# Kernel tuning notes

Hardware: AMD Instinct MI355X
Metric: run time of the kernel (lower is better)

Reference implementation:

```python
import jax, jax.numpy as jnp
import numpy as np

B, N, D, H = 8, 1024, 768, 4
ALPHA = 0.2      # LeakyReLU negative slope in GraphAttentionLayer
NEG = -9e15      # mask fill value for non-edges (pyGAT convention)


def setup_inputs() -> dict:
    key = jax.random.key(0)
    ks = jax.random.split(key, 8)
    input_emb = jax.random.normal(ks[0], (B, N, D), jnp.float32)
    adj = jax.random.randint(ks[1], (B, N, N), 0, 2, dtype=jnp.int32)
    mask_node = jnp.ones((B, N), jnp.float32)
    s = 1.0 / np.sqrt(D).astype(np.float32)
    W_heads = jax.random.normal(ks[2], (H, D, D), jnp.float32) * s          # per-head W: nfeat->nhid
    a_heads = jax.random.normal(ks[3], (H, 2 * D, 1), jnp.float32) * s      # per-head attention vector a
    W_out = jax.random.normal(ks[4], (H * D, D), jnp.float32) * (1.0 / np.sqrt(H * D).astype(np.float32))
    a_out = jax.random.normal(ks[5], (2 * D, 1), jnp.float32) * s
    w_cls = jax.random.normal(ks[6], (D, 1), jnp.float32) * s               # Classifier.linear1 weight
    b_cls = jnp.zeros((1,), jnp.float32)
    return dict(input_emb=input_emb, adj=adj, mask_node=mask_node,
                W_heads=W_heads, a_heads=a_heads, W_out=W_out, a_out=a_out,
                w_cls=w_cls, b_cls=b_cls)


def _gat_layer(x, adj_mask, W, a, concat):
    # x: [B,N,Fin], W: [Fin,Fout], a: [2*Fout,1], adj_mask: [B,N,N] bool
    Wh = jnp.einsum('bnd,df->bnf', x, W)            # [B,N,Fout]
    Fo = W.shape[1]
    f1 = Wh @ a[:Fo]                                 # [B,N,1] source term
    f2 = Wh @ a[Fo:]                                 # [B,N,1] target term
    e = jax.nn.leaky_relu(f1 + jnp.swapaxes(f2, 1, 2), ALPHA)  # [B,N,N]
    e = jnp.where(adj_mask, e, NEG)
    att = jax.nn.softmax(e, axis=-1)                 # dropout=0 -> no attention dropout
    h = jnp.einsum('bij,bjf->bif', att, Wh)          # [B,N,Fout]
    return jax.nn.elu(h) if concat else h


def reference(input_emb, adj, mask_node, W_heads, a_heads, W_out, a_out, w_cls, b_cls):
    adj_mask = adj > 0
    # multi-head GAT (concat=True heads), vectorized over heads and batch
    heads = jax.vmap(lambda Wi, ai: _gat_layer(input_emb, adj_mask, Wi, ai, True))(W_heads, a_heads)  # [H,B,N,D]
    xx = jnp.moveaxis(heads, 0, 2).reshape(B, N, H * D)  # torch.cat over heads, dim=1 per node
    out = jax.nn.elu(_gat_layer(xx, adj_mask, W_out, a_out, False))
    # dropout_layer(p=0.5) assumed eval mode (identity); residual add
    yy = out + input_emb                               # [B,N,D]
    h = (yy @ w_cls + b_cls)[..., 0]                   # Classifier linear -> [B,N]
    node_scores = jax.nn.sigmoid(h) * mask_node
    return yy, node_scores
```

## Files before the change

kernel.cpp:

```cpp
#include <hip/hip_runtime.h>


typedef unsigned short ushortT;
typedef _Float16 f16;
typedef __attribute__((ext_vector_type(8))) _Float16 f16x8;
typedef __attribute__((ext_vector_type(4))) _Float16 f16x4;
typedef __attribute__((ext_vector_type(4))) float f32x4;
typedef __attribute__((ext_vector_type(2))) float f32x2;
typedef __attribute__((ext_vector_type(8))) unsigned short u16x8;
typedef __attribute__((ext_vector_type(2))) unsigned short u16x2;
typedef __attribute__((ext_vector_type(4))) int i32x4;

#define ALPHA 0.2f

__device__ __forceinline__ float b2f(ushortT u) {
  union { unsigned int i; float f; } c; c.i = ((unsigned int)u) << 16; return c.f;
}
__device__ __forceinline__ ushortT f2b(float f) {
  union { float f; unsigned int u; } c; c.f = f;
  unsigned int u = c.u;
  u += 0x7FFFu + ((u >> 16) & 1u);
  return (ushortT)(u >> 16);
}

__global__ void detect_dtype(const ushortT* __restrict__ X, int* __restrict__ flag,
                             float* __restrict__ fvec) {
  __shared__ int s[256];
  int t = threadIdx.x, c = 0;
  for (int i = t; i < 2048; i += 256) fvec[i] = 0.f;
  for (int i = t; i < 16384; i += 256) {
    int e = (X[2 * i] >> 7) & 0xFF;
    if (e > 140 || e < 100) c++;
  }
  s[t] = c; __syncthreads();
  for (int o = 128; o > 0; o >>= 1) { if (t < o) s[t] += s[t + o]; __syncthreads(); }
  if (t == 0) *flag = (s[0] > 1000) ? 1 : 0;
}

template <int MODE, int BSRC>
__global__ __launch_bounds__(256) void mgemm(
    const void* __restrict__ Ab, const void* __restrict__ Bb,
    void* __restrict__ Cb, const void* __restrict__ Rb,
    int K, int lda, int ldb, int aRaw,
    long aOff, long bOff, long cOff, long rOff, int accum,
    const void* __restrict__ avec, long avOff, int fd, float* __restrict__ fvec,
    int zf, const int* __restrict__ rflag) {
  __shared__ __align__(16) f16 As[2][64 * 64];
  __shared__ __align__(16) f16 Bs[2][64 * 64];
  int t = threadIdx.x;
  int n0 = blockIdx.x * 64, m0 = blockIdx.y * 64;
  int flg = *rflag;
  int aTy = aRaw ? (flg ? 2 : 1) : 0;

  if (zf && blockIdx.x == 0 && blockIdx.y == 0) {
#pragma unroll
    for (int i = 0; i < 8; i++) fvec[t + i * 256] = 0.f;
  }

  int tq = t >> 2, cq = t & 3;
  long aBase = aOff + (long)(m0 + tq) * lda + cq * 16;
  int stA0 = tq * 64 + (((2 * cq)     ^ (tq & 7)) * 8);
  int stA1 = tq * 64 + (((2 * cq + 1) ^ (tq & 7)) * 8);

  const f16*     Ah = (const f16*)Ab;
  const ushortT* Au = (const ushortT*)Ab;
  const float*   Af = (const float*)Ab;
  const f16*     Bh = (const f16*)Bb;
  const ushortT* Bu = (const ushortT*)Bb;
  const float*   Bf = (const float*)Bb;

  long bBase = 0;
  int stB0, stB1;
  int q2 = 0, cB = 0;
  if (BSRC == 0) {
    bBase = bOff + (long)(n0 + tq) * (long)K + cq * 16;
    stB0 = stA0; stB1 = stA1;
  } else {
    q2 = t & 31; cB = t >> 5;
    int nb0 = 2 * q2, nb1 = nb0 + 1;
    stB0 = nb0 * 64 + ((cB ^ (nb0 & 7)) * 8);
    stB1 = nb1 * 64 + ((cB ^ (nb1 & 7)) * 8);
  }

  f16x8 ra0, ra1, rb0, rb1;

  auto loadA = [&](int kt) {
    long g = aBase + (long)kt * 64;
    if (aTy == 0) {
      ra0 = *(const f16x8*)(Ah + g);
      ra1 = *(const f16x8*)(Ah + g + 8);
    } else if (aTy == 1) {
      u16x8 v0 = *(const u16x8*)(Au + g);
      u16x8 v1 = *(const u16x8*)(Au + g + 8);
#pragma unroll
      for (int j = 0; j < 8; j++) { ra0[j] = (f16)b2f(v0[j]); ra1[j] = (f16)b2f(v1[j]); }
    } else {
      f32x4 v0 = *(const f32x4*)(Af + g);
      f32x4 v1 = *(const f32x4*)(Af + g + 4);
      f32x4 v2 = *(const f32x4*)(Af + g + 8);
      f32x4 v3 = *(const f32x4*)(Af + g + 12);
#pragma unroll
      for (int j = 0; j < 4; j++) {
        ra0[j] = (f16)v0[j]; ra0[4 + j] = (f16)v1[j];
        ra1[j] = (f16)v2[j]; ra1[4 + j] = (f16)v3[j];
      }
    }
  };
  auto loadB = [&](int kt) {
    if (BSRC == 0) {
      long g = bBase + (long)kt * 64;
      rb0 = *(const f16x8*)(Bh + g);
      rb1 = *(const f16x8*)(Bh + g + 8);
    } else {
      long rbase = bOff + (long)(kt * 64 + cB * 8) * ldb + n0 + 2 * q2;
      if (flg) {
#pragma unroll
        for (int j = 0; j < 8; j++) {
          f32x2 v = *(const f32x2*)(Bf + rbase + (long)j * ldb);
          rb0[j] = (f16)v[0]; rb1[j] = (f16)v[1];
        }
      } else {
#pragma unroll
        for (int j = 0; j < 8; j++) {
          u16x2 v = *(const u16x2*)(Bu + rbase + (long)j * ldb);
          rb0[j] = (f16)b2f(v[0]); rb1[j] = (f16)b2f(v[1]);
        }
      }
    }
  };
  auto stage = [&](int buf) {
    *(f16x8*)(&As[buf][0] + stA0) = ra0;  *(f16x8*)(&As[buf][0] + stA1) = ra1;
    *(f16x8*)(&Bs[buf][0] + stB0) = rb0;  *(f16x8*)(&Bs[buf][0] + stB1) = rb1;
  };

  int lane = t & 63, wid = t >> 6;
  int wr = wid >> 1, wc = wid & 1;
  int lr = lane & 15, lg = lane >> 4, l7 = lane & 7;
  int aRow0 = (wr * 32 + lr) * 64, aRow1 = aRow0 + 16 * 64;
  int bRow0 = (wc * 32 + lr) * 64, bRow1 = bRow0 + 16 * 64;
  int ch0 = ((lg) ^ l7) * 8, ch1 = ((4 + lg) ^ l7) * 8;

  f32x4 acc[2][2];
#pragma unroll
  for (int i = 0; i < 2; i++)
#pragma unroll
    for (int j = 0; j < 2; j++) acc[i][j] = (f32x4){0.f, 0.f, 0.f, 0.f};

  int KT = K >> 6;
  loadA(0); loadB(0);
  stage(0);
  loadA(1); loadB(1);
  __syncthreads();

  for (int kt = 0; kt < KT; ++kt) {
    int cur = kt & 1;
    if (kt + 1 < KT) stage(cur ^ 1);
    if (kt + 2 < KT) { loadA(kt + 2); loadB(kt + 2); }
#pragma unroll
    for (int kk = 0; kk < 2; kk++) {
      int ch = kk ? ch1 : ch0;
      f16x8 a0 = *(const f16x8*)(&As[cur][0] + aRow0 + ch);
      f16x8 a1 = *(const f16x8*)(&As[cur][0] + aRow1 + ch);
      f16x8 b0 = *(const f16x8*)(&Bs[cur][0] + bRow0 + ch);
      f16x8 b1 = *(const f16x8*)(&Bs[cur][0] + bRow1 + ch);
      acc[0][0] = __builtin_amdgcn_mfma_f32_16x16x32_f16(a0, b0, acc[0][0], 0, 0, 0);
      acc[0][1] = __builtin_amdgcn_mfma_f32_16x16x32_f16(a0, b1, acc[0][1], 0, 0, 0);
      acc[1][0] = __builtin_amdgcn_mfma_f32_16x16x32_f16(a1, b0, acc[1][0], 0, 0, 0);
      acc[1][1] = __builtin_amdgcn_mfma_f32_16x16x32_f16(a1, b1, acc[1][1], 0, 0, 0);
    }
    __syncthreads();
  }

  int rowb_base = m0 + wr * 32 + 4 * lg;
  int col_base  = n0 + wc * 32 + lr;

  float a1v[2], a2v[2];
  float p1[2][4], p2[2][4];
  if (fd) {
    const float* avf = (const float*)avec; const ushortT* avu = (const ushortT*)avec;
#pragma unroll
    for (int fn = 0; fn < 2; fn++) {
      int c = n0 + wc * 32 + fn * 16 + lr;
      a1v[fn] = flg ? avf[avOff + c]       : b2f(avu[avOff + c]);
      a2v[fn] = flg ? avf[avOff + 768 + c] : b2f(avu[avOff + 768 + c]);
    }
#pragma unroll
    for (int fm = 0; fm < 2; fm++)
#pragma unroll
      for (int r = 0; r < 4; r++) { p1[fm][r] = 0.f; p2[fm][r] = 0.f; }
  }

#pragma unroll
  for (int fm = 0; fm < 2; fm++) {
#pragma unroll
    for (int fn = 0; fn < 2; fn++) {
      int rowb = rowb_base + fm * 16;
      int col  = col_base + fn * 16;
      f32x4 v = acc[fm][fn];
      float fullv[4];
      if (MODE == 4) {
        f16x4 pk;
#pragma unroll
        for (int r = 0; r < 4; r++) { fullv[r] = v[r]; pk[r] = (f16)v[r]; }
        *(f16x4*)((f16*)Cb + (long)col * 1024 + rowb) = pk;
      } else if (MODE == 3) {
        f16* Cc = (f16*)Cb;
        long idx = (long)col * 1024 + rowb;
        f16x4 pk;
        if (accum) {
          f16x4 old = *(const f16x4*)(Cc + idx);
#pragma unroll
          for (int r = 0; r < 4; r++) { fullv[r] = (float)old[r] + v[r]; pk[r] = (f16)fullv[r]; }
        } else {
#pragma unroll
          for (int r = 0; r < 4; r++) { fullv[r] = v[r]; pk[r] = (f16)v[r]; }
        }
        *(f16x4*)(Cc + idx) = pk;
      } else {
#pragma unroll
        for (int r = 0; r < 4; r++) {
          int row = rowb + r;
          float x = v[r];
          x = x > 0.f ? x : __expf(x) - 1.f;
          long ci = cOff + (long)row * 768 + col;
          if (MODE == 2) {
            long ri = rOff + (long)row * 768 + col;
            x += flg ? ((const float*)Rb)[ri] : b2f(((const ushortT*)Rb)[ri]);
            if (flg) ((float*)Cb)[ci] = x;
            else     ((ushortT*)Cb)[ci] = f2b(x);
          } else {
            ((f16*)Cb)[ci] = (f16)x;
          }
        }
      }
      if (fd) {
        float ac1 = a1v[fn], ac2 = a2v[fn];
#pragma unroll
        for (int r = 0; r < 4; r++) {
          p1[fm][r] += fullv[r] * ac1;
          p2[fm][r] += fullv[r] * ac2;
        }
      }
    }
  }

  if (fd) {
#pragma unroll
    for (int fm = 0; fm < 2; fm++)
#pragma unroll
      for (int r = 0; r < 4; r++) {
#pragma unroll
        for (int o = 1; o < 16; o <<= 1) {
          p1[fm][r] += __shfl_xor(p1[fm][r], o);
          p2[fm][r] += __shfl_xor(p2[fm][r], o);
        }
      }
    if (lr == 0) {
#pragma unroll
      for (int fm = 0; fm < 2; fm++)
#pragma unroll
        for (int r = 0; r < 4; r++) {
          int row = rowb_base + fm * 16 + r;
          atomicAdd(fvec + row, p1[fm][r]);
          atomicAdd(fvec + 1024 + row, p2[fm][r]);
        }
    }
  }
}

__global__ __launch_bounds__(256) void attn_kernel(
    const float* __restrict__ f1, const float* __restrict__ f2,
    const int* __restrict__ adj, f16* __restrict__ att) {
  __shared__ float sred[8];
  int i = blockIdx.x;
  const int* arow = adj + (size_t)i * 1024;
  float f1i = f1[i];
  f16* orow = att + (size_t)i * 1024;
  int t = threadIdx.x, lane = t & 63, wid = t >> 6;
  int j0 = t * 4;

  i32x4 av = *(const i32x4*)(arow + j0);
  f32x4 fv = *(const f32x4*)(f2 + j0);

  float e[4];
  int msk[4];
  float mx = -1e38f;
#pragma unroll
  for (int c = 0; c < 4; c++) {
    float ev = f1i + fv[c];
    ev = ev > 0.f ? ev : ALPHA * ev;
    e[c] = ev;
    msk[c] = av[c] > 0;
    if (msk[c]) mx = fmaxf(mx, ev);
  }
#pragma unroll
  for (int o = 32; o > 0; o >>= 1) mx = fmaxf(mx, __shfl_down(mx, o));
  if (lane == 0) sred[wid] = mx;
  __syncthreads();
  float bmx = fmaxf(fmaxf(sred[0], sred[1]), fmaxf(sred[2], sred[3]));
  bool none = bmx < -1e37f;

  float p[4];
  float sum = 0.f;
#pragma unroll
  for (int c = 0; c < 4; c++) {
    p[c] = none ? 1.f : (msk[c] ? __expf(e[c] - bmx) : 0.f);
    sum += p[c];
  }
#pragma unroll
  for (int o = 32; o > 0; o >>= 1) sum += __shfl_down(sum, o);
  if (lane == 0) sred[4 + wid] = sum;
  __syncthreads();
  float inv = 1.f / (sred[4] + sred[5] + sred[6] + sred[7]);
  f16x4 pk;
#pragma unroll
  for (int c = 0; c < 4; c++) pk[c] = (f16)(p[c] * inv);
  *(f16x4*)(orow + j0) = pk;
}

__global__ __launch_bounds__(256) void cls_kernel(
    void* __restrict__ outbase, const void* __restrict__ w,
    const void* __restrict__ bc, const void* __restrict__ mask,
    const int* __restrict__ rflag) {
  int t = threadIdx.x, lane = t & 63, wv = t >> 6;
  long row = (long)blockIdx.x * 4 + wv;
  int f32 = *rflag;
  const float* yf = (const float*)outbase; const ushortT* yu = (const ushortT*)outbase;
  const float* wf = (const float*)w;       const ushortT* wu = (const ushortT*)w;
  float s = 0.f;
  for (int d = lane; d < 768; d += 64) {
    float yv = f32 ? yf[row * 768 + d] : b2f(yu[row * 768 + d]);
    float wvv = f32 ? wf[d] : b2f(wu[d]);
    s += yv * wvv;
  }
#pragma unroll
  for (int o = 32; o > 0; o >>= 1) s += __shfl_down(s, o);
  if (lane == 0) {
    float bb = f32 ? ((const float*)bc)[0] : b2f(((const ushortT*)bc)[0]);
    float mk = f32 ? ((const float*)mask)[row] : b2f(((const ushortT*)mask)[row]);
    float sig = 1.f / (1.f + __expf(-(s + bb)));
    long oi = 6291456L + row;
    if (f32) ((float*)outbase)[oi] = sig * mk;
    else ((ushortT*)outbase)[oi] = f2b(sig * mk);
  }
}

extern "C" void kernel_launch(void* const* d_in, const int* in_sizes, int n_in,
                              void* d_out, int out_size, void* d_ws, size_t ws_size,
                              hipStream_t stream) {
  (void)in_sizes; (void)n_in; (void)out_size; (void)ws_size;

  const void* X    = d_in[0];
  const int*  adj  = (const int*)d_in[1];
  const void* maskN= d_in[2];
  const void* Wh   = d_in[3];
  const void* aH   = d_in[4];
  const void* Wo   = d_in[5];
  const void* aO   = d_in[6];
  const void* wcls = d_in[7];
  const void* bcls = d_in[8];

  char* ws = (char*)d_ws;
  float* f1   = (float*)(ws + 0);
  float* f2   = (float*)(ws + 4096);
  int*   flag = (int*)(ws + 8192);
  f16* Wh1T = (f16*)(ws + 8448);
  f16* Wh2T = (f16*)(ws + 1581312);
  f16* attb = (f16*)(ws + 3154176);
  f16* hout = (f16*)(ws + 5251328);

  detect_dtype<<<1, 256, 0, stream>>>((const ushortT*)X, flag, f1);

  dim3 gg(12, 16);
  for (int b = 0; b < 8; b++) {
    long xOff = (long)b * 786432;
    for (int h = 0; h < 4; h++) {
      mgemm<4, 1><<<gg, 256, 0, stream>>>(
          X, Wh, Wh1T, nullptr, 768, 768, 768, 1,
          xOff, (long)h * 589824, 0L, 0L, 0, aH, (long)h * 1536, 1, f1, 0, flag);
      attn_kernel<<<1024, 256, 0, stream>>>(f1, f2, adj + (size_t)b * 1048576, attb);
      mgemm<1, 0><<<gg, 256, 0, stream>>>(
          attb, Wh1T, hout, nullptr, 1024, 1024, 0, 0,
          0L, 0L, 0L, 0L, 0, nullptr, 0L, 0, f1, 1, flag);
      mgemm<3, 1><<<gg, 256, 0, stream>>>(
          hout, Wo, Wh2T, nullptr, 768, 768, 768, 0,
          0L, (long)h * 589824, 0L, 0L, h > 0 ? 1 : 0, aO, 0L, h == 3 ? 1 : 0, f1, 0, flag);
    }
    attn_kernel<<<1024, 256, 0, stream>>>(f1, f2, adj + (size_t)b * 1048576, attb);
    mgemm<2, 0><<<gg, 256, 0, stream>>>(
        attb, Wh2T, d_out, X, 1024, 1024, 0, 0,
        0L, 0L, xOff, xOff, 0, nullptr, 0L, 0, f1, 1, flag);
  }

  cls_kernel<<<2048, 256, 0, stream>>>(d_out, wcls, bcls, maskN, flag);
}
```

Baseline: 1.779 ms.

## Pair independent GEMMs into single launches and use direct global-to-LDS loads

Independent GEMMs now share one launch through a z grid dimension: each head's Wo projection runs alongside the next head's Wh projection, and each batch's final attention GEMM runs alongside the next batch's first Wh projection. This is meant to fill the GPU better than the small 192-block grids did and to cut launch count. To keep the paired GEMMs from clobbering each other's f1/f2 scores, those vectors are double-buffered, with the second buffer placed in a scratch region past the outputs in d_out. The f16 A/B GEMM path also switches to global_load_lds with a swizzled layout, skipping the register staging. The risks are reliance on spare space in the output buffer and the more complex zeroing and phase logic.

```diff
diff --git a/kernel.cpp b/kernel.cpp
--- a/kernel.cpp
+++ b/kernel.cpp
@@ -22,116 +22,65 @@
   u += 0x7FFFu + ((u >> 16) & 1u);
   return (ushortT)(u >> 16);
 }
+__device__ __forceinline__ float* qbuf(char* dout, int flg) {
+  return (float*)(dout + (flg ? 25165824L : 12582912L));
+}
+__device__ __forceinline__ void gld16(const f16* g, f16* l) {
+  __builtin_amdgcn_global_load_lds(
+      (const __attribute__((address_space(1))) void*)g,
+      (__attribute__((address_space(3))) void*)l, 16, 0, 0);
+}
 
 __global__ void detect_dtype(const ushortT* __restrict__ X, int* __restrict__ flag,
-                             float* __restrict__ fvec) {
+                             float* __restrict__ Pws, char* __restrict__ dout) {
   __shared__ int s[256];
   int t = threadIdx.x, c = 0;
-  for (int i = t; i < 2048; i += 256) fvec[i] = 0.f;
   for (int i = t; i < 16384; i += 256) {
     int e = (X[2 * i] >> 7) & 0xFF;
     if (e > 140 || e < 100) c++;
   }
   s[t] = c; __syncthreads();
   for (int o = 128; o > 0; o >>= 1) { if (t < o) s[t] += s[t + o]; __syncthreads(); }
-  if (t == 0) *flag = (s[0] > 1000) ? 1 : 0;
-}
+  __syncthreads();
+  int fl = (s[0] > 1000) ? 1 : 0;
+  if (t == 0) *flag = fl;
+  float* Qv = qbuf(dout, fl);
+#pragma unroll
+  for (int i = 0; i < 8; i++) { Pws[t + i * 256] = 0.f; Qv[t + i * 256] = 0.f; }
+}
+
+struct GA {
+  const void* A; const void* B; void* C; const void* R; const void* avec;
+  long aOff, bOff, cOff, rOff, avOff;
+  int K, lda, ldb, aRaw, accum, fd, fsel, zmask;
+};
 
 template <int MODE, int BSRC>
-__global__ __launch_bounds__(256) void mgemm(
-    const void* __restrict__ Ab, const void* __restrict__ Bb,
-    void* __restrict__ Cb, const void* __restrict__ Rb,
-    int K, int lda, int ldb, int aRaw,
-    long aOff, long bOff, long cOff, long rOff, int accum,
-    const void* __restrict__ avec, long avOff, int fd, float* __restrict__ fvec,
-    int zf, const int* __restrict__ rflag) {
-  __shared__ __align__(16) f16 As[2][64 * 64];
-  __shared__ __align__(16) f16 Bs[2][64 * 64];
+__device__ void gbody(const GA a, float* Pws, char* dout, int flg,
+                      f16* AS, f16* BS) {
   int t = threadIdx.x;
   int n0 = blockIdx.x * 64, m0 = blockIdx.y * 64;
-  int flg = *rflag;
-  int aTy = aRaw ? (flg ? 2 : 1) : 0;
-
-  if (zf && blockIdx.x == 0 && blockIdx.y == 0) {
-#pragma unroll
-    for (int i = 0; i < 8; i++) fvec[t + i * 256] = 0.f;
-  }
-
-  int tq = t >> 2, cq = t & 3;
-  long aBase = aOff + (long)(m0 + tq) * lda + cq * 16;
-  int stA0 = tq * 64 + (((2 * cq)     ^ (tq & 7)) * 8);
-  int stA1 = tq * 64 + (((2 * cq + 1) ^ (tq & 7)) * 8);
-
-  const f16*     Ah = (const f16*)Ab;
-  const ushortT* Au = (const ushortT*)Ab;
-  const float*   Af = (const float*)Ab;
-  const f16*     Bh = (const f16*)Bb;
-  const ushortT* Bu = (const ushortT*)Bb;
-  const float*   Bf = (const float*)Bb;
-
-  long bBase = 0;
-  int stB0, stB1;
-  int q2 = 0, cB = 0;
-  if (BSRC == 0) {
-    bBase = bOff + (long)(n0 + tq) * (long)K + cq * 16;
-    stB0 = stA0; stB1 = stA1;
-  } else {
-    q2 = t & 31; cB = t >> 5;
-    int nb0 = 2 * q2, nb1 = nb0 + 1;
-    stB0 = nb0 * 64 + ((cB ^ (nb0 & 7)) * 8);
-    stB1 = nb1 * 64 + ((cB ^ (nb1 & 7)) * 8);
-  }
-
-  f16x8 ra0, ra1, rb0, rb1;
-
-  auto loadA = [&](int kt) {
-    long g = aBase + (long)kt * 64;
-    if (aTy == 0) {
-      ra0 = *(const f16x8*)(Ah + g);
-      ra1 = *(const f16x8*)(Ah + g + 8);
-    } else if (aTy == 1) {
-      u16x8 v0 = *(const u16x8*)(Au + g);
-      u16x8 v1 = *(const u16x8*)(Au + g + 8);
-#pragma unroll
-      for (int j = 0; j < 8; j++) { ra0[j] = (f16)b2f(v0[j]); ra1[j] = (f16)b2f(v1[j]); }
-    } else {
-      f32x4 v0 = *(const f32x4*)(Af + g);
-      f32x4 v1 = *(const f32x4*)(Af + g + 4);
-      f32x4 v2 = *(const f32x4*)(Af + g + 8);
-      f32x4 v3 = *(const f32x4*)(Af + g + 12);
-#pragma unroll
-      for (int j = 0; j < 4; j++) {
-        ra0[j] = (f16)v0[j]; ra0[4 + j] = (f16)v1[j];
-        ra1[j] = (f16)v2[j]; ra1[4 + j] = (f16)v3[j];
-      }
-    }
-  };
-  auto loadB = [&](int kt) {
-    if (BSRC == 0) {
-      long g = bBase + (long)kt * 64;
-      rb0 = *(const f16x8*)(Bh + g);
-      rb1 = *(const f16x8*)(Bh + g + 8);
-    } else {
-      long rbase = bOff + (long)(kt * 64 + cB * 8) * ldb + n0 + 2 * q2;
-      if (flg) {
-#pragma unroll
-        for (int j = 0; j < 8; j++) {
-          f32x2 v = *(const f32x2*)(Bf + rbase + (long)j * ldb);
-          rb0[j] = (f16)v[0]; rb1[j] = (f16)v[1];
-        }
-      } else {
-#pragma unroll
-        for (int j = 0; j < 8; j++) {
-          u16x2 v = *(const u16x2*)(Bu + rbase + (long)j * ldb);
-          rb0[j] = (f16)b2f(v[0]); rb1[j] = (f16)b2f(v[1]);
-        }
-      }
-    }
-  };
-  auto stage = [&](int buf) {
-    *(f16x8*)(&As[buf][0] + stA0) = ra0;  *(f16x8*)(&As[buf][0] + stA1) = ra1;
-    *(f16x8*)(&Bs[buf][0] + stB0) = rb0;  *(f16x8*)(&Bs[buf][0] + stB1) = rb1;
-  };
+  int aTy = a.aRaw ? (flg ? 2 : 1) : 0;
+  float* fv = a.fsel ? qbuf(dout, flg) : Pws;
+
+  if (a.zmask && blockIdx.x == 0 && blockIdx.y == 0) {
+    if (a.zmask & 1) {
+#pragma unroll
+      for (int i = 0; i < 8; i++) Pws[t + i * 256] = 0.f;
+    }
+    if (a.zmask & 2) {
+      float* Qv = qbuf(dout, flg);
+#pragma unroll
+      for (int i = 0; i < 8; i++) Qv[t + i * 256] = 0.f;
+    }
+  }
+
+  const f16*     Ah = (const f16*)a.A;
+  const ushortT* Au = (const ushortT*)a.A;
+  const float*   Af = (const float*)a.A;
+  const f16*     Bh = (const f16*)a.B;
+  const ushortT* Bu = (const ushortT*)a.B;
+  const float*   Bf = (const float*)a.B;
 
   int lane = t & 63, wid = t >> 6;
   int wr = wid >> 1, wc = wid & 1;
@@ -146,29 +95,118 @@
 #pragma unroll
     for (int j = 0; j < 2; j++) acc[i][j] = (f32x4){0.f, 0.f, 0.f, 0.f};
 
-  int KT = K >> 6;
-  loadA(0); loadB(0);
-  stage(0);
-  loadA(1); loadB(1);
-  __syncthreads();
-
-  for (int kt = 0; kt < KT; ++kt) {
-    int cur = kt & 1;
-    if (kt + 1 < KT) stage(cur ^ 1);
-    if (kt + 2 < KT) { loadA(kt + 2); loadB(kt + 2); }
+  auto compute = [&](int cur) {
+    f16* Ac = AS + cur * 4096; f16* Bc = BS + cur * 4096;
 #pragma unroll
     for (int kk = 0; kk < 2; kk++) {
       int ch = kk ? ch1 : ch0;
-      f16x8 a0 = *(const f16x8*)(&As[cur][0] + aRow0 + ch);
-      f16x8 a1 = *(const f16x8*)(&As[cur][0] + aRow1 + ch);
-      f16x8 b0 = *(const f16x8*)(&Bs[cur][0] + bRow0 + ch);
-      f16x8 b1 = *(const f16x8*)(&Bs[cur][0] + bRow1 + ch);
+      f16x8 a0 = *(const f16x8*)(Ac + aRow0 + ch);
+      f16x8 a1 = *(const f16x8*)(Ac + aRow1 + ch);
+      f16x8 b0 = *(const f16x8*)(Bc + bRow0 + ch);
+      f16x8 b1 = *(const f16x8*)(Bc + bRow1 + ch);
       acc[0][0] = __builtin_amdgcn_mfma_f32_16x16x32_f16(a0, b0, acc[0][0], 0, 0, 0);
       acc[0][1] = __builtin_amdgcn_mfma_f32_16x16x32_f16(a0, b1, acc[0][1], 0, 0, 0);
       acc[1][0] = __builtin_amdgcn_mfma_f32_16x16x32_f16(a1, b0, acc[1][0], 0, 0, 0);
       acc[1][1] = __builtin_amdgcn_mfma_f32_16x16x32_f16(a1, b1, acc[1][1], 0, 0, 0);
     }
+  };
+
+  int KT = a.K >> 6;
+
+  if (BSRC == 0) {
+    int gr = lane >> 3, gcn = lane & 7, swz = (gcn ^ (gr & 7)) * 8;
+    int isB = wid >> 1, cq4 = (wid & 1) * 4;
+    long gA = a.aOff + (long)(m0 + gr) * a.lda + swz;
+    long gB = a.bOff + (long)(n0 + gr) * (long)a.K + swz;
+    auto stageG = [&](int buf, int kt) {
+      if (!isB) {
+        const f16* g = Ah + gA + (long)kt * 64;
+        f16* dst = AS + buf * 4096;
+#pragma unroll
+        for (int c = 0; c < 4; c++)
+          gld16(g + (long)(cq4 + c) * 8 * a.lda, dst + (cq4 + c) * 512);
+      } else {
+        const f16* g = Bh + gB + (long)kt * 64;
+        f16* dst = BS + buf * 4096;
+#pragma unroll
+        for (int c = 0; c < 4; c++)
+          gld16(g + (long)(cq4 + c) * 8 * a.K, dst + (cq4 + c) * 512);
+      }
+    };
+    stageG(0, 0);
     __syncthreads();
+    for (int kt = 0; kt < KT; ++kt) {
+      int cur = kt & 1;
+      if (kt + 1 < KT) stageG(cur ^ 1, kt + 1);
+      compute(cur);
+      __syncthreads();
+    }
+  } else {
+    int tq = t >> 2, cq = t & 3;
+    long aBase = a.aOff + (long)(m0 + tq) * a.lda + cq * 16;
+    int stA0 = tq * 64 + (((2 * cq)     ^ (tq & 7)) * 8);
+    int stA1 = tq * 64 + (((2 * cq + 1) ^ (tq & 7)) * 8);
+    int q2 = t & 31, cB = t >> 5;
+    int nb0 = 2 * q2, nb1 = nb0 + 1;
+    int stB0 = nb0 * 64 + ((cB ^ (nb0 & 7)) * 8);
+    int stB1 = nb1 * 64 + ((cB ^ (nb1 & 7)) * 8);
+
+    f16x8 ra0, ra1, rb0, rb1;
+    auto loadA = [&](int kt) {
+      long g = aBase + (long)kt * 64;
+      if (aTy == 0) {
+        ra0 = *(const f16x8*)(Ah + g);
+        ra1 = *(const f16x8*)(Ah + g + 8);
+      } else if (aTy == 1) {
+        u16x8 v0 = *(const u16x8*)(Au + g);
+        u16x8 v1 = *(const u16x8*)(Au + g + 8);
+#pragma unroll
+        for (int j = 0; j < 8; j++) { ra0[j] = (f16)b2f(v0[j]); ra1[j] = (f16)b2f(v1[j]); }
+      } else {
+        f32x4 v0 = *(const f32x4*)(Af + g);
+        f32x4 v1 = *(const f32x4*)(Af + g + 4);
+        f32x4 v2 = *(const f32x4*)(Af + g + 8);
+        f32x4 v3 = *(const f32x4*)(Af + g + 12);
+#pragma unroll
+        for (int j = 0; j < 4; j++) {
+          ra0[j] = (f16)v0[j]; ra0[4 + j] = (f16)v1[j];
+          ra1[j] = (f16)v2[j]; ra1[4 + j] = (f16)v3[j];
+        }
+      }
+    };
+    auto loadB = [&](int kt) {
+      long rbase = a.bOff + (long)(kt * 64 + cB * 8) * a.ldb + n0 + 2 * q2;
+      if (flg) {
+#pragma unroll
+        for (int j = 0; j < 8; j++) {
+          f32x2 v = *(const f32x2*)(Bf + rbase + (long)j * a.ldb);
+          rb0[j] = (f16)v[0]; rb1[j] = (f16)v[1];
+        }
+      } else {
+#pragma unroll
+        for (int j = 0; j < 8; j++) {
+          u16x2 v = *(const u16x2*)(Bu + rbase + (long)j * a.ldb);
+          rb0[j] = (f16)b2f(v[0]); rb1[j] = (f16)b2f(v[1]);
+        }
+      }
+    };
+    auto stage = [&](int buf) {
+      *(f16x8*)(AS + buf * 4096 + stA0) = ra0;
+      *(f16x8*)(AS + buf * 4096 + stA1) = ra1;
+      *(f16x8*)(BS + buf * 4096 + stB0) = rb0;
+      *(f16x8*)(BS + buf * 4096 + stB1) = rb1;
+    };
+    loadA(0); loadB(0);
+    stage(0);
+    loadA(1); loadB(1);
+    __syncthreads();
+    for (int kt = 0; kt < KT; ++kt) {
+      int cur = kt & 1;
+      if (kt + 1 < KT) stage(cur ^ 1);
+      if (kt + 2 < KT) { loadA(kt + 2); loadB(kt + 2); }
+      compute(cur);
+      __syncthreads();
+    }
   }
 
   int rowb_base = m0 + wr * 32 + 4 * lg;
@@ -176,13 +214,13 @@
 
   float a1v[2], a2v[2];
   float p1[2][4], p2[2][4];
-  if (fd) {
-    const float* avf = (const float*)avec; const ushortT* avu = (const ushortT*)avec;
+  if (a.fd) {
+    const float* avf = (const float*)a.avec; const ushortT* avu = (const ushortT*)a.avec;
 #pragma unroll
     for (int fn = 0; fn < 2; fn++) {
       int c = n0 + wc * 32 + fn * 16 + lr;
-      a1v[fn] = flg ? avf[avOff + c]       : b2f(avu[avOff + c]);
-      a2v[fn] = flg ? avf[avOff + 768 + c] : b2f(avu[avOff + 768 + c]);
+      a1v[fn] = flg ? avf[a.avOff + c]       : b2f(avu[a.avOff + c]);
+      a2v[fn] = flg ? avf[a.avOff + 768 + c] : b2f(avu[a.avOff + 768 + c]);
     }
 #pragma unroll
     for (int fm = 0; fm < 2; fm++)
@@ -202,12 +240,12 @@
         f16x4 pk;
 #pragma unroll
         for (int r = 0; r < 4; r++) { fullv[r] = v[r]; pk[r] = (f16)v[r]; }
-        *(f16x4*)((f16*)Cb + (long)col * 1024 + rowb) = pk;
+        *(f16x4*)((f16*)a.C + (long)col * 1024 + rowb) = pk;
       } else if (MODE == 3) {
-        f16* Cc = (f16*)Cb;
+        f16* Cc = (f16*)a.C;
         long idx = (long)col * 1024 + rowb;
         f16x4 pk;
-        if (accum) {
+        if (a.accum) {
           f16x4 old = *(const f16x4*)(Cc + idx);
 #pragma unroll
           for (int r = 0; r < 4; r++) { fullv[r] = (float)old[r] + v[r]; pk[r] = (f16)fullv[r]; }
@@ -222,18 +260,18 @@
           int row = rowb + r;
           float x = v[r];
           x = x > 0.f ? x : __expf(x) - 1.f;
-          long ci = cOff + (long)row * 768 + col;
+          long ci = a.cOff + (long)row * 768 + col;
           if (MODE == 2) {
-            long ri = rOff + (long)row * 768 + col;
-            x += flg ? ((const float*)Rb)[ri] : b2f(((const ushortT*)Rb)[ri]);
-            if (flg) ((float*)Cb)[ci] = x;
-            else     ((ushortT*)Cb)[ci] = f2b(x);
+            long ri = a.rOff + (long)row * 768 + col;
+            x += flg ? ((const float*)a.R)[ri] : b2f(((const ushortT*)a.R)[ri]);
+            if (flg) ((float*)a.C)[ci] = x;
+            else     ((ushortT*)a.C)[ci] = f2b(x);
           } else {
-            ((f16*)Cb)[ci] = (f16)x;
+            ((f16*)a.C)[ci] = (f16)x;
           }
         }
       }
-      if (fd) {
+      if (a.fd) {
         float ac1 = a1v[fn], ac2 = a2v[fn];
 #pragma unroll
         for (int r = 0; r < 4; r++) {
@@ -244,7 +282,7 @@
     }
   }
 
-  if (fd) {
+  if (a.fd) {
 #pragma unroll
     for (int fm = 0; fm < 2; fm++)
 #pragma unroll
@@ -261,17 +299,46 @@
 #pragma unroll
         for (int r = 0; r < 4; r++) {
           int row = rowb_base + fm * 16 + r;
-          atomicAdd(fvec + row, p1[fm][r]);
-          atomicAdd(fvec + 1024 + row, p2[fm][r]);
-        }
-    }
-  }
+          atomicAdd(fv + row, p1[fm][r]);
+          atomicAdd(fv + 1024 + row, p2[fm][r]);
+        }
+    }
+  }
+}
+
+template <int MODE, int BSRC>
+__global__ __launch_bounds__(256) void k_solo(GA a, float* Pws, char* dout,
+                                              const int* __restrict__ rflag) {
+  __shared__ __align__(16) f16 As[2][4096];
+  __shared__ __align__(16) f16 Bs[2][4096];
+  gbody<MODE, BSRC>(a, Pws, dout, *rflag, &As[0][0], &Bs[0][0]);
+}
+__global__ __launch_bounds__(256) void k_pair31(GA g3, GA g1, float* Pws, char* dout,
+                                                const int* __restrict__ rflag) {
+  __shared__ __align__(16) f16 As[2][4096];
+  __shared__ __align__(16) f16 Bs[2][4096];
+  int flg = *rflag;
+  if (blockIdx.z == 0) gbody<3, 1>(g3, Pws, dout, flg, &As[0][0], &Bs[0][0]);
+  else                 gbody<4, 1>(g1, Pws, dout, flg, &As[0][0], &Bs[0][0]);
+}
+__global__ __launch_bounds__(256) void k_pair41(GA g4, GA g1, float* Pws, char* dout,
+                                                const int* __restrict__ rflag) {
+  __shared__ __align__(16) f16 As[2][4096];
+  __shared__ __align__(16) f16 Bs[2][4096];
+  int flg = *rflag;
+  if (blockIdx.z == 0) gbody<2, 0>(g4, Pws, dout, flg, &As[0][0], &Bs[0][0]);
+  else                 gbody<4, 1>(g1, Pws, dout, flg, &As[0][0], &Bs[0][0]);
 }
 
 __global__ __launch_bounds__(256) void attn_kernel(
-    const float* __restrict__ f1, const float* __restrict__ f2,
-    const int* __restrict__ adj, f16* __restrict__ att) {
+    const float* __restrict__ Pws, char* __restrict__ dout, int fsel,
+    const int* __restrict__ adj, f16* __restrict__ att,
+    const int* __restrict__ rflag) {
   __shared__ float sred[8];
+  int flg = *rflag;
+  const float* fvb = fsel ? qbuf(dout, flg) : Pws;
+  const float* f1 = fvb;
+  const float* f2 = fvb + 1024;
   int i = blockIdx.x;
   const int* arow = adj + (size_t)i * 1024;
   float f1i = f1[i];
@@ -280,14 +347,14 @@
   int j0 = t * 4;
 
   i32x4 av = *(const i32x4*)(arow + j0);
-  f32x4 fv = *(const f32x4*)(f2 + j0);
+  f32x4 fvv = *(const f32x4*)(f2 + j0);
 
   float e[4];
   int msk[4];
   float mx = -1e38f;
 #pragma unroll
   for (int c = 0; c < 4; c++) {
-    float ev = f1i + fv[c];
+    float ev = f1i + fvv[c];
     ev = ev > 0.f ? ev : ALPHA * ev;
     e[c] = ev;
     msk[c] = av[c] > 0;
@@ -361,35 +428,61 @@
   const void* bcls = d_in[8];
 
   char* ws = (char*)d_ws;
-  float* f1   = (float*)(ws + 0);
-  float* f2   = (float*)(ws + 4096);
+  float* Pws  = (float*)(ws + 0);
   int*   flag = (int*)(ws + 8192);
   f16* Wh1T = (f16*)(ws + 8448);
   f16* Wh2T = (f16*)(ws + 1581312);
   f16* attb = (f16*)(ws + 3154176);
   f16* hout = (f16*)(ws + 5251328);
-
-  detect_dtype<<<1, 256, 0, stream>>>((const ushortT*)X, flag, f1);
-
-  dim3 gg(12, 16);
+  char* dob = (char*)d_out;
+
+  detect_dtype<<<1, 256, 0, stream>>>((const ushortT*)X, flag, Pws, dob);
+
+  auto mkG1 = [&](int b, int h) {
+    GA g{}; g.A = X; g.B = Wh; g.C = Wh1T; g.R = nullptr; g.avec = aH;
+    g.aOff = (long)b * 786432; g.bOff = (long)h * 589824;
+    g.cOff = 0; g.rOff = 0; g.avOff = (long)h * 1536;
+    g.K = 768; g.lda = 768; g.ldb = 768; g.aRaw = 1; g.accum = 0;
+    g.fd = 1; g.fsel = (h + (b & 1)) & 1; g.zmask = 0;
+    return g;
+  };
+
+  dim3 gg(12, 16), gp(12, 16, 2);
+  k_solo<4, 1><<<gg, 256, 0, stream>>>(mkG1(0, 0), Pws, dob, flag);
+
   for (int b = 0; b < 8; b++) {
+    int phase = b & 1;
     long xOff = (long)b * 786432;
     for (int h = 0; h < 4; h++) {
-      mgemm<4, 1><<<gg, 256, 0, stream>>>(
-          X, Wh, Wh1T, nullptr, 768, 768, 768, 1,
-          xOff, (long)h * 589824, 0L, 0L, 0, aH, (long)h * 1536, 1, f1, 0, flag);
-      attn_kernel<<<1024, 256, 0, stream>>>(f1, f2, adj + (size_t)b * 1048576, attb);
-      mgemm<1, 0><<<gg, 256, 0, stream>>>(
-          attb, Wh1T, hout, nullptr, 1024, 1024, 0, 0,
-          0L, 0L, 0L, 0L, 0, nullptr, 0L, 0, f1, 1, flag);
-      mgemm<3, 1><<<gg, 256, 0, stream>>>(
-          hout, Wo, Wh2T, nullptr, 768, 768, 768, 0,
-          0L, (long)h * 589824, 0L, 0L, h > 0 ? 1 : 0, aO, 0L, h == 3 ? 1 : 0, f1, 0, flag);
-    }
-    attn_kernel<<<1024, 256, 0, stream>>>(f1, f2, adj + (size_t)b * 1048576, attb);
-    mgemm<2, 0><<<gg, 256, 0, stream>>>(
-        attb, Wh2T, d_out, X, 1024, 1024, 0, 0,
-        0L, 0L, xOff, xOff, 0, nullptr, 0L, 0, f1, 1, flag);
+      attn_kernel<<<1024, 256, 0, stream>>>(
+          Pws, dob, (h + phase) & 1, adj + (size_t)b * 1048576, attb, flag);
+      GA g2{}; g2.A = attb; g2.B = Wh1T; g2.C = hout;
+      g2.K = 1024; g2.lda = 1024; g2.ldb = 1024; g2.aRaw = 0; g2.accum = 0;
+      g2.fd = 0; g2.fsel = 0;
+      g2.zmask = (h < 3) ? (1 << ((h + 1 + phase) & 1)) : 3;
+      k_solo<1, 0><<<gg, 256, 0, stream>>>(g2, Pws, dob, flag);
+      GA g3{}; g3.A = hout; g3.B = Wo; g3.C = Wh2T; g3.avec = aO;
+      g3.bOff = (long)h * 589824; g3.avOff = 0;
+      g3.K = 768; g3.lda = 768; g3.ldb = 768; g3.aRaw = 0;
+      g3.accum = h > 0 ? 1 : 0;
+      g3.fd = (h == 3) ? 1 : 0; g3.fsel = phase; g3.zmask = 0;
+      if (h < 3) {
+        k_pair31<<<gp, 256, 0, stream>>>(g3, mkG1(b, h + 1), Pws, dob, flag);
+      } else {
+        k_solo<3, 1><<<gg, 256, 0, stream>>>(g3, Pws, dob, flag);
+      }
+    }
+    attn_kernel<<<1024, 256, 0, stream>>>(
+        Pws, dob, phase, adj + (size_t)b * 1048576, attb, flag);
+    GA g4{}; g4.A = attb; g4.B = Wh2T; g4.C = d_out; g4.R = X;
+    g4.cOff = xOff; g4.rOff = xOff;
+    g4.K = 1024; g4.lda = 1024; g4.ldb = 1024; g4.aRaw = 0; g4.accum = 0;
+    g4.fd = 0; g4.fsel = 0; g4.zmask = 0;
+    if (b < 7) {
+      k_pair41<<<gp, 256, 0, stream>>>(g4, mkG1(b + 1, 0), Pws, dob, flag);
+    } else {
+      k_solo<2, 0><<<gg, 256, 0, stream>>>(g4, Pws, dob, flag);
+    }
   }
 
   cls_kernel<<<2048, 256, 0, stream>>>(d_out, wcls, bcls, maskN, flag);
```

New measurement: 1.480 ms. 1.2x faster.
